# Optimization experiments

Measured on AMD Instinct MI355X. Metric: run time of the kernel, lower is better.

## Reference

```python
import jax, jax.numpy as jnp
import numpy as np

N_HEADS, D_MODEL, D_HEAD = 16, 1024, 64
INIT_STD = 0.02
IGNORE = -100000.0


def setup_inputs() -> dict:
    key = jax.random.key(0)
    ks = jax.random.split(key, 5)
    x = jax.random.normal(ks[0], (2, 2048, D_MODEL), dtype=jnp.float32)
    W_Q = INIT_STD * jax.random.normal(ks[1], (N_HEADS, D_MODEL, D_HEAD), dtype=jnp.float32)
    W_K = INIT_STD * jax.random.normal(ks[2], (N_HEADS, D_MODEL, D_HEAD), dtype=jnp.float32)
    W_V = INIT_STD * jax.random.normal(ks[3], (N_HEADS, D_MODEL, D_HEAD), dtype=jnp.float32)
    W_O = INIT_STD * jax.random.normal(ks[4], (N_HEADS, D_HEAD, D_MODEL), dtype=jnp.float32)
    b_Q = jnp.zeros((N_HEADS, D_HEAD), dtype=jnp.float32)
    b_K = jnp.zeros((N_HEADS, D_HEAD), dtype=jnp.float32)
    b_V = jnp.zeros((N_HEADS, D_HEAD), dtype=jnp.float32)
    b_O = jnp.zeros((D_MODEL,), dtype=jnp.float32)
    return {"normalized_resid_pre": x, "W_Q": W_Q, "W_K": W_K, "W_V": W_V,
            "W_O": W_O, "b_Q": b_Q, "b_K": b_K, "b_V": b_V, "b_O": b_O}


def reference(normalized_resid_pre, W_Q, W_K, W_V, W_O, b_Q, b_K, b_V, b_O):
    x = normalized_resid_pre  # [b, s, d_model]
    q = jnp.einsum('bsm,hmd->bshd', x, W_Q) + b_Q  # [b, s, h, d_head]
    k = jnp.einsum('bsm,hmd->bshd', x, W_K) + b_K
    v = jnp.einsum('bsm,hmd->bshd', x, W_V) + b_V
    scores = jnp.einsum('bqhd,bkhd->bhqk', q, k) / jnp.sqrt(jnp.float32(D_HEAD))
    s = x.shape[1]
    causal = jnp.triu(jnp.ones((s, s), dtype=bool), k=1)  # True above diagonal
    scores = jnp.where(causal, jnp.float32(IGNORE), scores)
    pattern = jax.nn.softmax(scores, axis=-1)  # [b, h, q, k]
    z = jnp.einsum('bkhd,bhqk->bqhd', v, pattern)
    attn_out = jnp.einsum('bqhd,hdm->bqm', z, W_O) + b_O
    return attn_out
```

## Files before the change

kernel.cpp:

```cpp
#include <hip/hip_runtime.h>
#include <hip/hip_bf16.h>

#define BB   2
#define SS   2048
#define HH   16
#define DM_  1024
#define DH_  64
#define NROW 4096
#define NQKV 3072

typedef unsigned short u16;
typedef unsigned int u32;
using short4v = __attribute__((ext_vector_type(4))) short;
using short8 = __attribute__((ext_vector_type(8))) short;
using bf16x8 = __attribute__((ext_vector_type(8))) __bf16;
using f32x4  = __attribute__((ext_vector_type(4))) float;
using f32x16 = __attribute__((ext_vector_type(16))) float;

#define QSCALE 0.180336880f

__device__ __forceinline__ u16 f2bf(float f) {
    union { float f; unsigned u; } v; v.f = f;
    unsigned r = v.u + 0x7fffu + ((v.u >> 16) & 1u);
    return (u16)(r >> 16);
}

__device__ __forceinline__ f32x4 mfma16(bf16x8 a, bf16x8 b, f32x4 c) {
    return __builtin_amdgcn_mfma_f32_16x16x32_bf16(a, b, c, 0, 0, 0);
}
__device__ __forceinline__ f32x16 mfma32(bf16x8 a, bf16x8 b, f32x16 c) {
    return __builtin_amdgcn_mfma_f32_32x32x16_bf16(a, b, c, 0, 0, 0);
}

__device__ __forceinline__ u32 cvtpk(float lo, float hi) {
    u32 r;
    asm("v_cvt_pk_bf16_f32 %0, %1, %2" : "=v"(r) : "v"(lo), "v"(hi));
    return r;
}
#define PLSWAP(a, b) asm("v_permlane32_swap_b32 %0, %1" : "+v"(a), "+v"(b))

__device__ __forceinline__ float fexp2(float x) {
#if __has_builtin(__builtin_amdgcn_exp2f)
    return __builtin_amdgcn_exp2f(x);
#else
    float r; asm("v_exp_f32 %0, %1" : "=v"(r) : "v"(x)); return r;
#endif
}

__device__ __forceinline__ void gload16(const void* g, void* l) {
    __builtin_amdgcn_global_load_lds(
        (const __attribute__((address_space(1))) void*)g,
        (__attribute__((address_space(3))) void*)l, 16, 0, 0);
}

__global__ __launch_bounds__(256)
void prep(const float* __restrict__ x,  const float* __restrict__ wq,
          const float* __restrict__ wk, const float* __restrict__ wv,
          const float* __restrict__ wo, const float* __restrict__ bq,
          const float* __restrict__ bk, const float* __restrict__ bv,
          u16* __restrict__ Xb, u16* __restrict__ Wt,
          u16* __restrict__ WoT, float* __restrict__ biasQKV) {
    __shared__ float tile[64][65];
    const int bx = blockIdx.x, t = threadIdx.x;
    if (bx < 512) {
        const int tid = bx * 256 + t;
        #pragma unroll
        for (int it = 0; it < 8; ++it) {
            int i = tid + it * 131072;
            float4 v = ((const float4*)x)[i];
            u16 b4[4] = {f2bf(v.x), f2bf(v.y), f2bf(v.z), f2bf(v.w)};
            ((short4v*)Xb)[i] = *(short4v*)b4;
        }
        if (tid < NQKV) {
            int mat = tid >> 10, h = (tid >> 6) & 15, d = tid & 63;
            const float* bb = (mat == 0) ? bq : ((mat == 1) ? bk : bv);
            biasQKV[tid] = bb[h * DH_ + d];
        }
    } else if (bx < 1280) {
        const int idx = bx - 512;
        const int m0 = (idx & 15) * 64, hm = idx >> 4;
        const int mat = hm >> 4, h = hm & 15;
        const float* w = (mat == 0) ? wq : ((mat == 1) ? wk : wv);
        #pragma unroll
        for (int it = 0; it < 4; ++it) {
            int row = it * 16 + (t >> 4), c4 = (t & 15) * 4;
            float4 v = *(const float4*)&w[((size_t)h * 1024 + m0 + row) * 64 + c4];
            tile[row][c4] = v.x; tile[row][c4 + 1] = v.y;
            tile[row][c4 + 2] = v.z; tile[row][c4 + 3] = v.w;
        }
        __syncthreads();
        #pragma unroll
        for (int it = 0; it < 2; ++it) {
            int c = it * 256 + t, d = c >> 3, mc = (c & 7) * 8;
            u16 buf[8];
            #pragma unroll
            for (int j = 0; j < 8; ++j) buf[j] = f2bf(tile[mc + j][d]);
            *(short8*)&Wt[((size_t)(mat * 1024 + h * 64 + d)) * 1024 + m0 + mc] = *(short8*)buf;
        }
    } else {
        const int idx = bx - 1280;
        const int n0 = (idx & 15) * 64, k0 = (idx >> 4) * 64;
        #pragma unroll
        for (int it = 0; it < 4; ++it) {
            int row = it * 16 + (t >> 4), c4 = (t & 15) * 4;
            float4 v = *(const float4*)&wo[(size_t)(k0 + row) * DM_ + n0 + c4];
            tile[row][c4] = v.x; tile[row][c4 + 1] = v.y;
            tile[row][c4 + 2] = v.z; tile[row][c4 + 3] = v.w;
        }
        __syncthreads();
        #pragma unroll
        for (int it = 0; it < 2; ++it) {
            int c = it * 256 + t, n = c >> 3, kc = (c & 7) * 8;
            u16 buf[8];
            #pragma unroll
            for (int j = 0; j < 8; ++j) buf[j] = f2bf(tile[kc + j][n]);
            *(short8*)&WoT[(size_t)(n0 + n) * DM_ + k0 + kc] = *(short8*)buf;
        }
    }
}

__device__ __forceinline__ void gemm_core_128(
    const u16* __restrict__ Ap, const u16* __restrict__ Bp,
    int brow, int bcol, u16* lds, f32x4 acc[4][2]) {
    const int t = threadIdx.x, l = t & 63;
    const int wid = t >> 6, wm = wid >> 2, wn = wid & 3;
    const int c0 = t, c1 = t + 512;
    const int r0 = c0 >> 3, sb0 = ((c0 & 7) ^ (r0 & 7)) << 3;
    const int r1 = c1 >> 3, sb1 = ((c1 & 7) ^ (r1 & 7)) << 3;
    u16* A0 = lds;
    u16* B0 = lds + 16384;
    const int rA0 = wm * 64 + (l & 15);
    const int rB0 = wn * 32 + (l & 15);
    const int sw  = (l & 7) << 3;
    const int colA = ((l >> 4) << 3);

    {
        gload16(Ap + (size_t)(brow + r0) * DM_ + sb0, A0 + c0 * 8);
        gload16(Ap + (size_t)(brow + r1) * DM_ + sb1, A0 + c1 * 8);
        gload16(Bp + (size_t)(bcol + r0) * DM_ + sb0, B0 + c0 * 8);
        gload16(Bp + (size_t)(bcol + r1) * DM_ + sb1, B0 + c1 * 8);
    }
    __syncthreads();
    for (int kt = 0; kt < 16; ++kt) {
        const int p = kt & 1;
        if (kt < 15) {
            const int ko = (kt + 1) * 64;
            gload16(Ap + (size_t)(brow + r0) * DM_ + ko + sb0, A0 + (p ^ 1) * 8192 + c0 * 8);
            gload16(Ap + (size_t)(brow + r1) * DM_ + ko + sb1, A0 + (p ^ 1) * 8192 + c1 * 8);
            gload16(Bp + (size_t)(bcol + r0) * DM_ + ko + sb0, B0 + (p ^ 1) * 8192 + c0 * 8);
            gload16(Bp + (size_t)(bcol + r1) * DM_ + ko + sb1, B0 + (p ^ 1) * 8192 + c1 * 8);
        }
        const u16* Ab = A0 + p * 8192;
        const u16* Bb = B0 + p * 8192;
        #pragma unroll
        for (int kc = 0; kc < 64; kc += 32) {
            const int cx = (kc + colA) ^ sw;
            bf16x8 af[4], bfr[2];
            #pragma unroll
            for (int m = 0; m < 4; ++m)
                af[m] = *(const bf16x8*)(Ab + (rA0 + m * 16) * 64 + cx);
            #pragma unroll
            for (int n = 0; n < 2; ++n)
                bfr[n] = *(const bf16x8*)(Bb + (rB0 + n * 16) * 64 + cx);
            __builtin_amdgcn_s_setprio(1);
            #pragma unroll
            for (int m = 0; m < 4; ++m)
                #pragma unroll
                for (int n = 0; n < 2; ++n)
                    acc[m][n] = mfma16(af[m], bfr[n], acc[m][n]);
            __builtin_amdgcn_s_setprio(0);
        }
        __syncthreads();
    }
}

__global__ __launch_bounds__(512)
void gemm_qkv3(const u16* __restrict__ Xb, const u16* __restrict__ Wt,
               const float* __restrict__ bias, u16* __restrict__ Qs,
               u16* __restrict__ Ks, u16* __restrict__ Vt) {
    __shared__ __align__(16) u16 lds[32768];
    const int bx = blockIdx.x, t = threadIdx.x, l = t & 63;
    const int wid = t >> 6, wm = wid >> 2, wn = wid & 3;
    f32x4 acc[4][2] = {};
    const bool isV = (bx >= 512);
    int brow, bcol; const u16 *Ap, *Bp;
    if (!isV) { brow = (bx & 31) * 128; bcol = (bx >> 5) * 128; Ap = Xb; Bp = Wt; }
    else { int i2 = bx - 512; brow = (i2 & 7) * 128; bcol = (i2 >> 3) * 128;
           Ap = Wt + (size_t)2048 * DM_; Bp = Xb; }
    gemm_core_128(Ap, Bp, brow, bcol, lds, acc);

    u16* wr_ = lds + wid * 2048;
    const int colbase = bcol + wn * 32;
    const int rowbase = brow + wm * 64;
    const int rsub = ((l >> 4) << 2);
    if (!isV) {
        const float b0 = bias[colbase + (l & 15)];
        const float b1 = bias[colbase + 16 + (l & 15)];
        const float scl = (colbase < 1024) ? QSCALE : 1.0f;
        #pragma unroll
        for (int m = 0; m < 4; ++m)
            #pragma unroll
            for (int n = 0; n < 2; ++n) {
                const float bb = n ? b1 : b0;
                #pragma unroll
                for (int r = 0; r < 4; ++r)
                    wr_[(m * 16 + rsub + r) * 32 + n * 16 + (l & 15)] =
                        f2bf((acc[m][n][r] + bb) * scl);
            }
    } else {
        #pragma unroll
        for (int m = 0; m < 4; ++m) {
            float4 bv = *(const float4*)&bias[2048 + rowbase + m * 16 + rsub];
            const float bbr[4] = {bv.x, bv.y, bv.z, bv.w};
            #pragma unroll
            for (int n = 0; n < 2; ++n)
                #pragma unroll
                for (int r = 0; r < 4; ++r)
                    wr_[(m * 16 + rsub + r) * 32 + n * 16 + (l & 15)] =
                        f2bf(acc[m][n][r] + bbr[r]);
        }
    }
    __syncthreads();
    if (!isV) {
        const int hsel = (colbase >> 6) & 15, d0 = colbase & 63;
        const int bsel = rowbase >> 11, s0 = rowbase & 2047;
        u16* outp = (colbase < 1024) ? Qs : Ks;
        #pragma unroll
        for (int p = 0; p < 4; ++p) {
            const int rr = p * 16 + (l >> 2);
            short8 v = *(const short8*)(wr_ + rr * 32 + (l & 3) * 8);
            *(short8*)&outp[(((size_t)bsel * HH + hsel) * SS + s0 + rr) * DH_ + d0 + (l & 3) * 8] = v;
        }
    } else {
        const int bsel = colbase >> 11, s0 = colbase & 2047;
        #pragma unroll
        for (int p = 0; p < 4; ++p) {
            const int rr = p * 16 + (l >> 2);
            short8 v = *(const short8*)(wr_ + rr * 32 + (l & 3) * 8);
            *(short8*)&Vt[((size_t)bsel * 1024 + rowbase + rr) * SS + s0 + (l & 3) * 8] = v;
        }
    }
}

__global__ __launch_bounds__(512)
void gemm_out3(const u16* __restrict__ Zb, const u16* __restrict__ WoT,
               const float* __restrict__ bO, float* __restrict__ out) {
    __shared__ __align__(16) u16 lds[32768];
    const int bx = blockIdx.x, t = threadIdx.x, l = t & 63;
    const int wid = t >> 6, wm = wid >> 2, wn = wid & 3;
    const int brow = (bx & 31) * 128, bcol = (bx >> 5) * 128;
    f32x4 acc[4][2] = {};
    gemm_core_128(Zb, WoT, brow, bcol, lds, acc);
    const int colbase = bcol + wn * 32;
    const int rowbase = brow + wm * 64;
    const int rsub = ((l >> 4) << 2);
    const float b0 = bO[colbase + (l & 15)];
    const float b1 = bO[colbase + 16 + (l & 15)];
    #pragma unroll
    for (int m = 0; m < 4; ++m)
        #pragma unroll
        for (int n = 0; n < 2; ++n) {
            const float bb = n ? b1 : b0;
            #pragma unroll
            for (int r = 0; r < 4; ++r)
                out[(size_t)(rowbase + m * 16 + rsub + r) * DM_ + colbase + n * 16 + (l & 15)] =
                    acc[m][n][r] + bb;
        }
}

__global__ __launch_bounds__(256, 4)
void attn_fwd(const u16* __restrict__ Qs, const u16* __restrict__ Ks,
              const u16* __restrict__ Vt, u16* __restrict__ Zb) {
    __shared__ __align__(16) u16 fKV[16384];
    __shared__ __align__(16) float lrP[64];
    __shared__ __align__(16) float lrX[64];
    const int bidx = blockIdx.x;
    const int a  = bidx >> 5;
    const int bh = bidx & 31, b = bh >> 4, h = bh & 15;
    const int t = threadIdx.x, wid = t >> 6, l = t & 63;
    const int hi = l >> 5, c32 = l & 31;
    const int qh = wid >> 1, par = wid & 1;
    const u16* Qp = Qs + (size_t)bh * SS * DH_;
    const u16* Kp = Ks + (size_t)bh * SS * DH_;
    const u16* Vp = Vt + (size_t)bh * DH_ * SS;

    int kOff[2]; size_t vOff[2]; int dstc[2];
    #pragma unroll
    for (int i = 0; i < 2; ++i) {
        const int c = t + 256 * i, sec = c >> 6, ln = c & 63;
        kOff[i] = ((sec >> 2) * 32 + (ln & 31)) * DH_ + (sec & 3) * 16 + (ln >> 5) * 8;
        vOff[i] = (size_t)((sec >> 2) * 32 + (ln & 31)) * SS + (sec & 3) * 16 + (ln >> 5) * 8;
        dstc[i] = c * 8;
    }
    u16* fK0 = fKV;          u16* fK1 = fKV + 4096;
    u16* fV0 = fKV + 8192;   u16* fV1 = fKV + 12288;
    const u16* fKb = par ? fK1 : fK0;
    const u16* fVb = par ? fV1 : fV0;

    #pragma unroll
    for (int ph = 0; ph < 2; ++ph) {
        const int qt = ph ? (31 - a) : a;
        const int qw = qt * 64 + qh * 32;
        const int nr = (qt >> 1) + 1;

        bf16x8 aq[4];
        #pragma unroll
        for (int dk = 0; dk < 4; ++dk)
            aq[dk] = *(const bf16x8*)&Qp[(size_t)(qw + c32) * DH_ + dk * 16 + hi * 8];

        f32x16 o0 = {}, o1 = {};
        float lrp[4] = {0.f, 0.f, 0.f, 0.f};

        for (int r = 0; r < nr; ++r) {
            const int k0a = r * 128, k0b = r * 128 + 64;
            __syncthreads();
            #pragma unroll
            for (int i = 0; i < 2; ++i) {
                gload16(Kp + (size_t)k0a * DH_ + kOff[i], fK0 + dstc[i]);
                gload16(Kp + (size_t)k0b * DH_ + kOff[i], fK1 + dstc[i]);
                gload16(Vp + k0a + vOff[i], fV0 + dstc[i]);
                gload16(Vp + k0b + vOff[i], fV1 + dstc[i]);
            }
            __syncthreads();
            const int kv0 = r * 128 + par * 64;
            if (kv0 <= qw + 31) {
                const bool have1 = (kv0 + 32 <= qw + 31);
                f32x16 s0 = {}, s1 = {};
                __builtin_amdgcn_s_setprio(1);
                #pragma unroll
                for (int dk = 0; dk < 4; ++dk)
                    s0 = mfma32(*(const bf16x8*)(fKb + dk * 512 + l * 8), aq[dk], s0);
                if (have1) {
                    #pragma unroll
                    for (int dk = 0; dk < 4; ++dk)
                        s1 = mfma32(*(const bf16x8*)(fKb + (4 + dk) * 512 + l * 8), aq[dk], s1);
                }
                __builtin_amdgcn_s_setprio(0);
                if (kv0 + 63 > qw) {
                    const int q = qw + c32;
                    #pragma unroll
                    for (int r16 = 0; r16 < 16; ++r16) {
                        const int crow = (r16 & 3) + 8 * (r16 >> 2) + 4 * hi;
                        if (kv0 + crow > q) s0[r16] = -1e30f;
                    }
                    if (have1) {
                        #pragma unroll
                        for (int r16 = 0; r16 < 16; ++r16) {
                            const int crow = (r16 & 3) + 8 * (r16 >> 2) + 4 * hi;
                            if (kv0 + 32 + crow > q) s1[r16] = -1e30f;
                        }
                    }
                }
                #pragma unroll
                for (int r16 = 0; r16 < 16; ++r16) {
                    s0[r16] = fexp2(s0[r16]);
                    lrp[r16 & 3] += s0[r16];
                }
                if (have1) {
                    #pragma unroll
                    for (int r16 = 0; r16 < 16; ++r16) {
                        s1[r16] = fexp2(s1[r16]);
                        lrp[r16 & 3] += s1[r16];
                    }
                }
                __builtin_amdgcn_s_setprio(1);
                #define PV_STEP(PS, B8, KS)                                          \
                {                                                                    \
                    u32 cA  = cvtpk(PS[B8 + 0], PS[B8 + 1]);                         \
                    u32 cA2 = cvtpk(PS[B8 + 2], PS[B8 + 3]);                         \
                    u32 cB  = cvtpk(PS[B8 + 4], PS[B8 + 5]);                         \
                    u32 cB2 = cvtpk(PS[B8 + 6], PS[B8 + 7]);                         \
                    PLSWAP(cA, cB); PLSWAP(cA2, cB2);                                \
                    u32 w[4] = {cA, cA2, cB, cB2};                                   \
                    bf16x8 pa = *(bf16x8*)w;                                         \
                    o0 = mfma32(pa, *(const bf16x8*)(fVb + (0 * 4 + (KS)) * 512 + l * 8), o0); \
                    o1 = mfma32(pa, *(const bf16x8*)(fVb + (1 * 4 + (KS)) * 512 + l * 8), o1); \
                }
                PV_STEP(s0, 0, 0)
                PV_STEP(s0, 8, 1)
                if (have1) {
                    PV_STEP(s1, 0, 2)
                    PV_STEP(s1, 8, 3)
                }
                #undef PV_STEP
                __builtin_amdgcn_s_setprio(0);
            }
        }

        float lrow = (lrp[0] + lrp[1]) + (lrp[2] + lrp[3]);
        lrow += __shfl_xor(lrow, 32);

        float* mrg = (float*)fKV;
        __syncthreads();
        if (par) {
            #pragma unroll
            for (int e = 0; e < 16; ++e) mrg[qh * 2048 + e * 64 + l] = o0[e];
            #pragma unroll
            for (int e = 0; e < 16; ++e) mrg[qh * 2048 + (16 + e) * 64 + l] = o1[e];
            if (hi == 0) lrP[qh * 32 + c32] = lrow;
        }
        __syncthreads();
        if (!par) {
            #pragma unroll
            for (int e = 0; e < 16; ++e) o0[e] += mrg[qh * 2048 + e * 64 + l];
            #pragma unroll
            for (int e = 0; e < 16; ++e) o1[e] += mrg[qh * 2048 + (16 + e) * 64 + l];
            lrow += lrP[qh * 32 + c32];
            lrX[qh * 32 + c32] = lrow;
            float invv[16];
            #pragma unroll
            for (int g = 0; g < 4; ++g) {
                float4 lv = *(const float4*)&lrX[qh * 32 + 8 * g + 4 * hi];
                invv[g * 4 + 0] = 1.0f / lv.x;
                invv[g * 4 + 1] = 1.0f / lv.y;
                invv[g * 4 + 2] = 1.0f / lv.z;
                invv[g * 4 + 3] = 1.0f / lv.w;
            }
            #pragma unroll
            for (int r16 = 0; r16 < 16; ++r16) {
                const int q = qw + (r16 & 3) + 8 * (r16 >> 2) + 4 * hi;
                u16* zp = &Zb[(((size_t)b * SS + q) * HH + h) * DH_];
                zp[c32]      = f2bf(o0[r16] * invv[r16]);
                zp[32 + c32] = f2bf(o1[r16] * invv[r16]);
            }
        }
    }
}

extern "C" void kernel_launch(void* const* d_in, const int* in_sizes, int n_in,
                              void* d_out, int out_size, void* d_ws, size_t ws_size,
                              hipStream_t stream) {
    const float* x  = (const float*)d_in[0];
    const float* wq = (const float*)d_in[1];
    const float* wk = (const float*)d_in[2];
    const float* wv = (const float*)d_in[3];
    const float* wo = (const float*)d_in[4];
    const float* bq = (const float*)d_in[5];
    const float* bk = (const float*)d_in[6];
    const float* bv = (const float*)d_in[7];
    const float* bO = (const float*)d_in[8];
    float* out = (float*)d_out;

    char* w = (char*)d_ws;
    u16* Xb  = (u16*)w;  w += (size_t)NROW * DM_ * 2;
    u16* Wt  = (u16*)w;  w += (size_t)NQKV * DM_ * 2;
    u16* WoT = (u16*)w;  w += (size_t)DM_ * DM_ * 2;
    float* biasQKV = (float*)w; w += (size_t)NQKV * 4;
    u16* Qs  = (u16*)w;  w += (size_t)BB * HH * SS * DH_ * 2;
    u16* Ks  = (u16*)w;  w += (size_t)BB * HH * SS * DH_ * 2;
    u16* Vt  = (u16*)w;  w += (size_t)BB * HH * SS * DH_ * 2;
    u16* Zb  = (u16*)w;  w += (size_t)BB * HH * SS * DH_ * 2;

    prep<<<1536, 256, 0, stream>>>(x, wq, wk, wv, wo, bq, bk, bv,
                                   Xb, Wt, WoT, biasQKV);
    gemm_qkv3<<<768, 512, 0, stream>>>(Xb, Wt, biasQKV, Qs, Ks, Vt);
    attn_fwd<<<512, 256, 0, stream>>>(Qs, Ks, Vt, Zb);
    gemm_out3<<<256, 512, 0, stream>>>(Zb, WoT, bO, out);
}
```

Baseline: 97.93 us.

## Split attention KV range over four waves per query half, drop tile pairing

The attention kernel moves from 256-thread blocks that each handle a paired early and late query tile to 512-thread blocks that each handle one query tile. Blocks are ordered longest-first so the heaviest causal tiles launch early. Four waves now split each 256-key chunk instead of two waves splitting a 128-key chunk, and the partial outputs are merged through a larger shared buffer. This aims to add parallelism and to halve the number of barrier-separated load steps per tile. In exchange, shared memory doubles (64KB K/V plus merge space), which may limit how many blocks fit per CU, and the cross-wave reduction does more work.

```diff
diff --git a/kernel.cpp b/kernel.cpp
--- a/kernel.cpp
+++ b/kernel.cpp
@@ -268,161 +268,161 @@
         }
 }
 
-__global__ __launch_bounds__(256, 4)
+__global__ __launch_bounds__(512, 4)
 void attn_fwd(const u16* __restrict__ Qs, const u16* __restrict__ Ks,
               const u16* __restrict__ Vt, u16* __restrict__ Zb) {
-    __shared__ __align__(16) u16 fKV[16384];
-    __shared__ __align__(16) float lrP[64];
+    __shared__ __align__(16) u16 fKV[32768];
+    __shared__ __align__(16) float lrP[256];
     __shared__ __align__(16) float lrX[64];
+    u16* fK = fKV;
+    u16* fV = fKV + 16384;
     const int bidx = blockIdx.x;
-    const int a  = bidx >> 5;
+    const int j  = 31 - (bidx >> 5);
     const int bh = bidx & 31, b = bh >> 4, h = bh & 15;
     const int t = threadIdx.x, wid = t >> 6, l = t & 63;
     const int hi = l >> 5, c32 = l & 31;
-    const int qh = wid >> 1, par = wid & 1;
+    const int qh = wid >> 2, par = wid & 3;
     const u16* Qp = Qs + (size_t)bh * SS * DH_;
     const u16* Kp = Ks + (size_t)bh * SS * DH_;
     const u16* Vp = Vt + (size_t)bh * DH_ * SS;
-
-    int kOff[2]; size_t vOff[2]; int dstc[2];
+    const int qw = j * 64 + qh * 32;
+    const int nr = (j >> 2) + 1;
+
+    bf16x8 aq[4];
     #pragma unroll
-    for (int i = 0; i < 2; ++i) {
-        const int c = t + 256 * i, sec = c >> 6, ln = c & 63;
-        kOff[i] = ((sec >> 2) * 32 + (ln & 31)) * DH_ + (sec & 3) * 16 + (ln >> 5) * 8;
-        vOff[i] = (size_t)((sec >> 2) * 32 + (ln & 31)) * SS + (sec & 3) * 16 + (ln >> 5) * 8;
+    for (int dk = 0; dk < 4; ++dk)
+        aq[dk] = *(const bf16x8*)&Qp[(size_t)(qw + c32) * DH_ + dk * 16 + hi * 8];
+
+    int kOff[4]; size_t vOff[4]; int dstc[4];
+    #pragma unroll
+    for (int i = 0; i < 4; ++i) {
+        const int c = t + 512 * i, sec = c >> 6, ln = c & 63;
+        kOff[i] = ((sec >> 3) * 64 + ((sec >> 2) & 1) * 32 + (ln & 31)) * DH_
+                  + (sec & 3) * 16 + (ln >> 5) * 8;
+        vOff[i] = (size_t)(((sec >> 2) & 1) * 32 + (ln & 31)) * SS
+                  + (sec >> 3) * 64 + (sec & 3) * 16 + (ln >> 5) * 8;
         dstc[i] = c * 8;
     }
-    u16* fK0 = fKV;          u16* fK1 = fKV + 4096;
-    u16* fV0 = fKV + 8192;   u16* fV1 = fKV + 12288;
-    const u16* fKb = par ? fK1 : fK0;
-    const u16* fVb = par ? fV1 : fV0;
-
-    #pragma unroll
-    for (int ph = 0; ph < 2; ++ph) {
-        const int qt = ph ? (31 - a) : a;
-        const int qw = qt * 64 + qh * 32;
-        const int nr = (qt >> 1) + 1;
-
-        bf16x8 aq[4];
-        #pragma unroll
-        for (int dk = 0; dk < 4; ++dk)
-            aq[dk] = *(const bf16x8*)&Qp[(size_t)(qw + c32) * DH_ + dk * 16 + hi * 8];
-
-        f32x16 o0 = {}, o1 = {};
-        float lrp[4] = {0.f, 0.f, 0.f, 0.f};
-
-        for (int r = 0; r < nr; ++r) {
-            const int k0a = r * 128, k0b = r * 128 + 64;
-            __syncthreads();
-            #pragma unroll
-            for (int i = 0; i < 2; ++i) {
-                gload16(Kp + (size_t)k0a * DH_ + kOff[i], fK0 + dstc[i]);
-                gload16(Kp + (size_t)k0b * DH_ + kOff[i], fK1 + dstc[i]);
-                gload16(Vp + k0a + vOff[i], fV0 + dstc[i]);
-                gload16(Vp + k0b + vOff[i], fV1 + dstc[i]);
-            }
-            __syncthreads();
-            const int kv0 = r * 128 + par * 64;
-            if (kv0 <= qw + 31) {
-                const bool have1 = (kv0 + 32 <= qw + 31);
-                f32x16 s0 = {}, s1 = {};
-                __builtin_amdgcn_s_setprio(1);
+    const u16* fKb = fK + par * 4096;
+    const u16* fVb = fV + par * 4096;
+
+    f32x16 o0 = {}, o1 = {};
+    float lrp[4] = {0.f, 0.f, 0.f, 0.f};
+
+    for (int r = 0; r < nr; ++r) {
+        const int k0a = r * 256;
+        __syncthreads();
+        #pragma unroll
+        for (int i = 0; i < 4; ++i) {
+            gload16(Kp + (size_t)k0a * DH_ + kOff[i], fK + dstc[i]);
+            gload16(Vp + k0a + vOff[i], fV + dstc[i]);
+        }
+        __syncthreads();
+        const int kv0 = k0a + par * 64;
+        if (kv0 <= qw + 31) {
+            const bool have1 = (kv0 + 32 <= qw + 31);
+            f32x16 s0 = {}, s1 = {};
+            __builtin_amdgcn_s_setprio(1);
+            #pragma unroll
+            for (int dk = 0; dk < 4; ++dk)
+                s0 = mfma32(*(const bf16x8*)(fKb + dk * 512 + l * 8), aq[dk], s0);
+            if (have1) {
                 #pragma unroll
                 for (int dk = 0; dk < 4; ++dk)
-                    s0 = mfma32(*(const bf16x8*)(fKb + dk * 512 + l * 8), aq[dk], s0);
-                if (have1) {
-                    #pragma unroll
-                    for (int dk = 0; dk < 4; ++dk)
-                        s1 = mfma32(*(const bf16x8*)(fKb + (4 + dk) * 512 + l * 8), aq[dk], s1);
-                }
-                __builtin_amdgcn_s_setprio(0);
-                if (kv0 + 63 > qw) {
-                    const int q = qw + c32;
-                    #pragma unroll
-                    for (int r16 = 0; r16 < 16; ++r16) {
-                        const int crow = (r16 & 3) + 8 * (r16 >> 2) + 4 * hi;
-                        if (kv0 + crow > q) s0[r16] = -1e30f;
-                    }
-                    if (have1) {
-                        #pragma unroll
-                        for (int r16 = 0; r16 < 16; ++r16) {
-                            const int crow = (r16 & 3) + 8 * (r16 >> 2) + 4 * hi;
-                            if (kv0 + 32 + crow > q) s1[r16] = -1e30f;
-                        }
-                    }
-                }
+                    s1 = mfma32(*(const bf16x8*)(fKb + (4 + dk) * 512 + l * 8), aq[dk], s1);
+            }
+            __builtin_amdgcn_s_setprio(0);
+            if (kv0 + 63 > qw) {
+                const int q = qw + c32;
                 #pragma unroll
                 for (int r16 = 0; r16 < 16; ++r16) {
-                    s0[r16] = fexp2(s0[r16]);
-                    lrp[r16 & 3] += s0[r16];
+                    const int crow = (r16 & 3) + 8 * (r16 >> 2) + 4 * hi;
+                    if (kv0 + crow > q) s0[r16] = -1e30f;
                 }
                 if (have1) {
                     #pragma unroll
                     for (int r16 = 0; r16 < 16; ++r16) {
-                        s1[r16] = fexp2(s1[r16]);
-                        lrp[r16 & 3] += s1[r16];
+                        const int crow = (r16 & 3) + 8 * (r16 >> 2) + 4 * hi;
+                        if (kv0 + 32 + crow > q) s1[r16] = -1e30f;
                     }
                 }
-                __builtin_amdgcn_s_setprio(1);
-                #define PV_STEP(PS, B8, KS)                                          \
-                {                                                                    \
-                    u32 cA  = cvtpk(PS[B8 + 0], PS[B8 + 1]);                         \
-                    u32 cA2 = cvtpk(PS[B8 + 2], PS[B8 + 3]);                         \
-                    u32 cB  = cvtpk(PS[B8 + 4], PS[B8 + 5]);                         \
-                    u32 cB2 = cvtpk(PS[B8 + 6], PS[B8 + 7]);                         \
-                    PLSWAP(cA, cB); PLSWAP(cA2, cB2);                                \
-                    u32 w[4] = {cA, cA2, cB, cB2};                                   \
-                    bf16x8 pa = *(bf16x8*)w;                                         \
-                    o0 = mfma32(pa, *(const bf16x8*)(fVb + (0 * 4 + (KS)) * 512 + l * 8), o0); \
-                    o1 = mfma32(pa, *(const bf16x8*)(fVb + (1 * 4 + (KS)) * 512 + l * 8), o1); \
+            }
+            #pragma unroll
+            for (int r16 = 0; r16 < 16; ++r16) {
+                s0[r16] = fexp2(s0[r16]);
+                lrp[r16 & 3] += s0[r16];
+            }
+            if (have1) {
+                #pragma unroll
+                for (int r16 = 0; r16 < 16; ++r16) {
+                    s1[r16] = fexp2(s1[r16]);
+                    lrp[r16 & 3] += s1[r16];
                 }
-                PV_STEP(s0, 0, 0)
-                PV_STEP(s0, 8, 1)
-                if (have1) {
-                    PV_STEP(s1, 0, 2)
-                    PV_STEP(s1, 8, 3)
-                }
-                #undef PV_STEP
-                __builtin_amdgcn_s_setprio(0);
-            }
-        }
-
-        float lrow = (lrp[0] + lrp[1]) + (lrp[2] + lrp[3]);
-        lrow += __shfl_xor(lrow, 32);
-
-        float* mrg = (float*)fKV;
-        __syncthreads();
-        if (par) {
-            #pragma unroll
-            for (int e = 0; e < 16; ++e) mrg[qh * 2048 + e * 64 + l] = o0[e];
-            #pragma unroll
-            for (int e = 0; e < 16; ++e) mrg[qh * 2048 + (16 + e) * 64 + l] = o1[e];
-            if (hi == 0) lrP[qh * 32 + c32] = lrow;
-        }
-        __syncthreads();
-        if (!par) {
-            #pragma unroll
-            for (int e = 0; e < 16; ++e) o0[e] += mrg[qh * 2048 + e * 64 + l];
-            #pragma unroll
-            for (int e = 0; e < 16; ++e) o1[e] += mrg[qh * 2048 + (16 + e) * 64 + l];
-            lrow += lrP[qh * 32 + c32];
-            lrX[qh * 32 + c32] = lrow;
-            float invv[16];
-            #pragma unroll
-            for (int g = 0; g < 4; ++g) {
-                float4 lv = *(const float4*)&lrX[qh * 32 + 8 * g + 4 * hi];
-                invv[g * 4 + 0] = 1.0f / lv.x;
-                invv[g * 4 + 1] = 1.0f / lv.y;
-                invv[g * 4 + 2] = 1.0f / lv.z;
-                invv[g * 4 + 3] = 1.0f / lv.w;
-            }
-            #pragma unroll
-            for (int r16 = 0; r16 < 16; ++r16) {
-                const int q = qw + (r16 & 3) + 8 * (r16 >> 2) + 4 * hi;
-                u16* zp = &Zb[(((size_t)b * SS + q) * HH + h) * DH_];
-                zp[c32]      = f2bf(o0[r16] * invv[r16]);
-                zp[32 + c32] = f2bf(o1[r16] * invv[r16]);
-            }
+            }
+            __builtin_amdgcn_s_setprio(1);
+            #define PV_STEP(PS, B8, KS)                                          \
+            {                                                                    \
+                u32 cA  = cvtpk(PS[B8 + 0], PS[B8 + 1]);                         \
+                u32 cA2 = cvtpk(PS[B8 + 2], PS[B8 + 3]);                         \
+                u32 cB  = cvtpk(PS[B8 + 4], PS[B8 + 5]);                         \
+                u32 cB2 = cvtpk(PS[B8 + 6], PS[B8 + 7]);                         \
+                PLSWAP(cA, cB); PLSWAP(cA2, cB2);                                \
+                u32 w[4] = {cA, cA2, cB, cB2};                                   \
+                bf16x8 pa = *(bf16x8*)w;                                         \
+                o0 = mfma32(pa, *(const bf16x8*)(fVb + (0 * 4 + (KS)) * 512 + l * 8), o0); \
+                o1 = mfma32(pa, *(const bf16x8*)(fVb + (1 * 4 + (KS)) * 512 + l * 8), o1); \
+            }
+            PV_STEP(s0, 0, 0)
+            PV_STEP(s0, 8, 1)
+            if (have1) {
+                PV_STEP(s1, 0, 2)
+                PV_STEP(s1, 8, 3)
+            }
+            #undef PV_STEP
+            __builtin_amdgcn_s_setprio(0);
+        }
+    }
+
+    float lrow = (lrp[0] + lrp[1]) + (lrp[2] + lrp[3]);
+    lrow += __shfl_xor(lrow, 32);
+
+    float* mrg = (float*)fKV;
+    __syncthreads();
+    if (par) {
+        float* m = mrg + ((qh * 3 + par - 1) << 11);
+        #pragma unroll
+        for (int e = 0; e < 16; ++e) m[e * 64 + l] = o0[e];
+        #pragma unroll
+        for (int e = 0; e < 16; ++e) m[(16 + e) * 64 + l] = o1[e];
+        if (hi == 0) lrP[(qh * 4 + par) * 32 + c32] = lrow;
+    }
+    __syncthreads();
+    if (!par) {
+        #pragma unroll
+        for (int pp = 1; pp < 4; ++pp) {
+            float* m = mrg + ((qh * 3 + pp - 1) << 11);
+            #pragma unroll
+            for (int e = 0; e < 16; ++e) o0[e] += m[e * 64 + l];
+            #pragma unroll
+            for (int e = 0; e < 16; ++e) o1[e] += m[(16 + e) * 64 + l];
+            lrow += lrP[(qh * 4 + pp) * 32 + c32];
+        }
+        lrX[qh * 32 + c32] = lrow;
+        float invv[16];
+        #pragma unroll
+        for (int g = 0; g < 4; ++g) {
+            float4 lv = *(const float4*)&lrX[qh * 32 + 8 * g + 4 * hi];
+            invv[g * 4 + 0] = 1.0f / lv.x;
+            invv[g * 4 + 1] = 1.0f / lv.y;
+            invv[g * 4 + 2] = 1.0f / lv.z;
+            invv[g * 4 + 3] = 1.0f / lv.w;
+        }
+        #pragma unroll
+        for (int r16 = 0; r16 < 16; ++r16) {
+            const int q = qw + (r16 & 3) + 8 * (r16 >> 2) + 4 * hi;
+            u16* zp = &Zb[(((size_t)b * SS + q) * HH + h) * DH_];
+            zp[c32]      = f2bf(o0[r16] * invv[r16]);
+            zp[32 + c32] = f2bf(o1[r16] * invv[r16]);
         }
     }
 }
@@ -454,6 +454,6 @@
     prep<<<1536, 256, 0, stream>>>(x, wq, wk, wv, wo, bq, bk, bv,
                                    Xb, Wt, WoT, biasQKV);
     gemm_qkv3<<<768, 512, 0, stream>>>(Xb, Wt, biasQKV, Qs, Ks, Vt);
-    attn_fwd<<<512, 256, 0, stream>>>(Qs, Ks, Vt, Zb);
+    attn_fwd<<<1024, 512, 0, stream>>>(Qs, Ks, Vt, Zb);
     gemm_out3<<<256, 512, 0, stream>>>(Zb, WoT, bO, out);
 }
```

Result: slower. 102.2 us (+4.4%).
